# Optimization experiments

Hardware: AMD Instinct MI355X
Metric: run time of the kernel (lower is better)

The kernel has to match this reference:

```python
import jax, jax.numpy as jnp
import numpy as np

N_LETTERS = 256
EMBED_DIM = 1024
HIDDEN_DIM = 2048
SEQ_LEN = 4096


def setup_inputs() -> dict:
    key = jax.random.key(0)
    ks = jax.random.split(key, 8)
    s_e = 1.0 / np.sqrt(EMBED_DIM)
    s_h = 1.0 / np.sqrt(HIDDEN_DIM)
    return {
        "input_ids": jax.random.randint(ks[0], (SEQ_LEN,), 0, N_LETTERS, dtype=jnp.int64)
        if jax.config.jax_enable_x64 else jax.random.randint(ks[0], (SEQ_LEN,), 0, N_LETTERS, dtype=jnp.int32),
        "h0": jnp.zeros((1, 1, HIDDEN_DIM), jnp.float32),
        "c0": jnp.zeros((1, 1, HIDDEN_DIM), jnp.float32),
        "W_emb": jax.random.normal(ks[1], (N_LETTERS, EMBED_DIM), jnp.float32),
        "W_ih": jax.random.normal(ks[2], (4 * HIDDEN_DIM, EMBED_DIM), jnp.float32) * s_e,
        "W_hh": jax.random.normal(ks[3], (4 * HIDDEN_DIM, HIDDEN_DIM), jnp.float32) * s_h,
        "b_ih": jnp.zeros((4 * HIDDEN_DIM,), jnp.float32),
        "b_hh": jnp.zeros((4 * HIDDEN_DIM,), jnp.float32),
        "W_out": jax.random.normal(ks[4], (N_LETTERS, HIDDEN_DIM), jnp.float32) * s_h,
        "b_out": jnp.zeros((N_LETTERS,), jnp.float32),
    }


def reference(input_ids, h0, c0, W_emb, W_ih, W_hh, b_ih, b_hh, W_out, b_out):
    H = W_hh.shape[1]
    emb = W_emb[input_ids]                       # [L, E]
    # Precompute the input-side gate projections for all timesteps (batched GEMM).
    x_gates = emb @ W_ih.T + (b_ih + b_hh)       # [L, 4H]

    def step(carry, xg):
        h, c = carry                             # [H], [H]
        gates = xg + W_hh @ h                    # [4H], PyTorch order i,f,g,o
        i = jax.nn.sigmoid(gates[0 * H:1 * H])
        f = jax.nn.sigmoid(gates[1 * H:2 * H])
        g = jnp.tanh(gates[2 * H:3 * H])
        o = jax.nn.sigmoid(gates[3 * H:4 * H])
        c_new = f * c + i * g
        h_new = o * jnp.tanh(c_new)
        return (h_new, c_new), h_new

    (hL, cL), hs = jax.lax.scan(step, (h0[0, 0], c0[0, 0]), x_gates)  # hs: [L, H]
    logits = hs @ W_out.T + b_out                # [L, n_letters]
    # Dropout(p=0.1) is identity in eval mode.
    out = jax.nn.log_softmax(jax.nn.relu(logits), axis=-1)
    return out, hL[None, None, :], cL[None, None, :]
```

## Files before the change

kernel.cpp:

```cpp
#include <hip/hip_runtime.h>
#include <hip/hip_bf16.h>

#define SEQ 4096
#define EMB 1024
#define HID 2048
#define G4  8192
#define NL  256

typedef __attribute__((ext_vector_type(8))) short bf16x8;
typedef __attribute__((ext_vector_type(4))) float f32x4;

static __device__ __forceinline__ unsigned short f2bf(float f) {
    unsigned int x = __builtin_bit_cast(unsigned int, f);
    return (unsigned short)((x + 0x7FFFu + ((x >> 16) & 1u)) >> 16);
}
static __device__ __forceinline__ float bf2f(unsigned short u) {
    return __builtin_bit_cast(float, ((unsigned int)u) << 16);
}
static __device__ __forceinline__ unsigned long long aload(const unsigned long long* p) {
    return __hip_atomic_load(p, __ATOMIC_RELAXED, __HIP_MEMORY_SCOPE_AGENT);
}
static __device__ __forceinline__ float fsigm(float x) {
    return 1.f / (1.f + __expf(-x));
}
static __device__ __forceinline__ float ftanh(float x) {
    return 1.f - 2.f / (__expf(2.f * x) + 1.f);
}

__global__ __launch_bounds__(256) void k_f2b(const float* __restrict__ in,
                                             unsigned short* __restrict__ out, int n) {
    int i = (blockIdx.x * 256 + threadIdx.x) * 4;
    if (i < n) {
        float4 v = *(const float4*)&in[i];
        ushort4 u;
        u.x = f2bf(v.x); u.y = f2bf(v.y); u.z = f2bf(v.z); u.w = f2bf(v.w);
        *(ushort4*)&out[i] = u;
    }
}

__global__ __launch_bounds__(256) void k_emb(const int* __restrict__ ids,
                                             const float* __restrict__ W_emb,
                                             unsigned short* __restrict__ out) {
    int t = blockIdx.x;
    int e0 = threadIdx.x * 4;
    const float4 v = *(const float4*)&W_emb[(size_t)ids[t] * EMB + e0];
    ushort4 u;
    u.x = f2bf(v.x); u.y = f2bf(v.y); u.z = f2bf(v.z); u.w = f2bf(v.w);
    *(ushort4*)&out[(size_t)t * EMB + e0] = u;
}

#define BM 128
#define BN 128
#define BK 32
__global__ __launch_bounds__(256) void k_gemm_bt(
    const unsigned short* __restrict__ A, const unsigned short* __restrict__ B,
    const float* __restrict__ bias1, const float* __restrict__ bias2,
    float* __restrict__ Cf, unsigned short* __restrict__ Cb,
    int M, int N, int K)
{
    __shared__ unsigned short As[BM * BK];
    __shared__ unsigned short Bs[BN * BK];
    const int bm = blockIdx.x * BM;
    const int bn = blockIdx.y * BN;
    const int tid = threadIdx.x;
    const int wave = tid >> 6, lane = tid & 63;
    const int wm = (wave & 1) * 64, wn = (wave >> 1) * 64;
    const int row16 = lane & 15, quad = lane >> 4;

    f32x4 acc[4][4];
#pragma unroll
    for (int i = 0; i < 4; ++i)
#pragma unroll
        for (int j = 0; j < 4; ++j) acc[i][j] = (f32x4){0.f, 0.f, 0.f, 0.f};

    for (int k0 = 0; k0 < K; k0 += BK) {
        __syncthreads();
#pragma unroll
        for (int s = 0; s < 2; ++s) {
            int c = tid + s * 256;
            int r = c >> 2, col = (c & 3) * 8;
            *(uint4*)&As[r * BK + col] = *(const uint4*)&A[(size_t)(bm + r) * K + k0 + col];
            *(uint4*)&Bs[r * BK + col] = *(const uint4*)&B[(size_t)(bn + r) * K + k0 + col];
        }
        __syncthreads();
        bf16x8 af[4], bfr[4];
#pragma unroll
        for (int i = 0; i < 4; ++i) {
            af[i]  = *(const bf16x8*)&As[(wm + i * 16 + row16) * BK + quad * 8];
            bfr[i] = *(const bf16x8*)&Bs[(wn + i * 16 + row16) * BK + quad * 8];
        }
#pragma unroll
        for (int i = 0; i < 4; ++i)
#pragma unroll
            for (int j = 0; j < 4; ++j)
                acc[i][j] = __builtin_amdgcn_mfma_f32_16x16x32_bf16(af[i], bfr[j], acc[i][j], 0, 0, 0);
    }

#pragma unroll
    for (int j = 0; j < 4; ++j) {
        int col = bn + wn + j * 16 + row16;
        float bsum = (bias1 ? bias1[col] : 0.f) + (bias2 ? bias2[col] : 0.f);
#pragma unroll
        for (int i = 0; i < 4; ++i) {
#pragma unroll
            for (int r = 0; r < 4; ++r) {
                int row = bm + wm + i * 16 + quad * 4 + r;
                float v = acc[i][j][r] + bsum;
                if (Cf) Cf[(size_t)row * N + col] = v;
                else    Cb[(size_t)row * N + col] = f2bf(v);
            }
        }
    }
}

#define LSTM_LDS 90112
__global__ __launch_bounds__(1024, 1) void k_lstm(
    const unsigned short* __restrict__ Whhb,
    const unsigned short* __restrict__ xg,
    const float* __restrict__ h0, const float* __restrict__ c0,
    unsigned short* __restrict__ hsb,
    float* __restrict__ outHC,
    unsigned long long* __restrict__ hcomm)
{
    extern __shared__ char smem[];
    float* LDSp = (float*)smem;

    const int b = blockIdx.x, tid = threadIdx.x;
    const int wave = tid >> 6, lane = tid & 63;
    const int sub = lane & 15, quad = lane >> 4;

    bf16x8 afr[4][4];
#pragma unroll
    for (int q = 0; q < 4; ++q) {
        const unsigned short* wsrc =
            Whhb + ((size_t)(q * HID + b * 16 + sub)) * HID + wave * 128 + quad * 8;
#pragma unroll
        for (int c = 0; c < 4; ++c)
            afr[q][c] = *(const bf16x8*)(wsrc + c * 32);
    }

    float creg = 0.f;
    if (tid < 16) creg = c0[b * 16 + tid];

    for (int t = 0; t < SEQ; ++t) {
        float xq0 = 0.f, xq1 = 0.f, xq2 = 0.f, xq3 = 0.f;
        if (wave == 0 && lane < 16) {
            const unsigned short* xr = xg + (size_t)t * G4 + b * 16 + lane;
            xq0 = bf2f(xr[0]);
            xq1 = bf2f(xr[2048]);
            xq2 = bf2f(xr[4096]);
            xq3 = bf2f(xr[6144]);
        }

        f32x4 acc[4];
#pragma unroll
        for (int q = 0; q < 4; ++q) acc[q] = (f32x4){0.f, 0.f, 0.f, 0.f};

        if (t == 0) {
#pragma unroll
            for (int c = 0; c < 4; ++c) {
                const float* hp = h0 + wave * 128 + c * 32 + quad * 8;
                float4 va = *(const float4*)hp;
                float4 vb = *(const float4*)(hp + 4);
                uint4 d;
                d.x = (unsigned)f2bf(va.x) | ((unsigned)f2bf(va.y) << 16);
                d.y = (unsigned)f2bf(va.z) | ((unsigned)f2bf(va.w) << 16);
                d.z = (unsigned)f2bf(vb.x) | ((unsigned)f2bf(vb.y) << 16);
                d.w = (unsigned)f2bf(vb.z) | ((unsigned)f2bf(vb.w) << 16);
                bf16x8 hf = __builtin_bit_cast(bf16x8, d);
#pragma unroll
                for (int q = 0; q < 4; ++q)
                    acc[q] = __builtin_amdgcn_mfma_f32_16x16x32_bf16(afr[q][c], hf, acc[q], 0, 0, 0);
            }
        } else {
            const unsigned long long* src =
                hcomm + (size_t)((t - 1) & 1) * 8192 + (size_t)(b & 7) * 1024 + wave * 64;
            const unsigned tag = (unsigned)t;
            if (wave != 0) __builtin_amdgcn_s_sleep(10);
            unsigned long long x;
            for (;;) {
                x = aload(&src[lane]);
                if ((unsigned)(x >> 32) == tag) break;
                __builtin_amdgcn_s_sleep(2);
            }
            int myd = (int)(unsigned)x;
#pragma unroll
            for (int c = 0; c < 4; ++c) {
                const int sl = c * 16 + quad * 4;
                uint4 d;
                d.x = (unsigned)__shfl(myd, sl + 0);
                d.y = (unsigned)__shfl(myd, sl + 1);
                d.z = (unsigned)__shfl(myd, sl + 2);
                d.w = (unsigned)__shfl(myd, sl + 3);
                bf16x8 hf = __builtin_bit_cast(bf16x8, d);
#pragma unroll
                for (int q = 0; q < 4; ++q)
                    acc[q] = __builtin_amdgcn_mfma_f32_16x16x32_bf16(afr[q][c], hf, acc[q], 0, 0, 0);
            }
        }

        float* P = LDSp + (t & 1) * 1100;
        if (sub == 0) {
#pragma unroll
            for (int q = 0; q < 4; ++q)
#pragma unroll
                for (int r = 0; r < 4; ++r)
                    P[(q * 16 + quad * 4 + r) * 17 + wave] = acc[q][r];
        }
        __syncthreads();

        if (wave == 0) {
            const float* rp = P + lane * 17;
            float g = 0.f;
#pragma unroll
            for (int i = 0; i < 16; ++i) g += rp[i];
            float gF = __shfl(g, lane + 16);
            float gG = __shfl(g, lane + 32);
            float gO = __shfl(g, lane + 48);
            unsigned hv = 0;
            float cn = 0.f, hn = 0.f;
            if (lane < 16) {
                float gi = g  + xq0;
                float gf = gF + xq1;
                float gg = gG + xq2;
                float go = gO + xq3;
                float i_ = fsigm(gi);
                float f_ = fsigm(gf);
                float g_ = ftanh(gg);
                float o_ = fsigm(go);
                cn = f_ * creg + i_ * g_;
                hn = o_ * ftanh(cn);
                creg = cn;
                hv = (unsigned)f2bf(hn);
            }
            {
                int j8 = lane & 7;
                unsigned lo = (unsigned)__shfl((int)hv, 2 * j8);
                unsigned hi = (unsigned)__shfl((int)hv, 2 * j8 + 1);
                unsigned long long wrd =
                    (((unsigned long long)(unsigned)(t + 1)) << 32)
                    | (unsigned long long)(lo | (hi << 16));
                __hip_atomic_store(
                    &hcomm[(size_t)(t & 1) * 8192 + (size_t)(lane >> 3) * 1024 + b * 8 + j8],
                    wrd, __ATOMIC_RELAXED, __HIP_MEMORY_SCOPE_AGENT);
            }
            if (lane < 16) {
                hsb[(size_t)t * HID + b * 16 + lane] = (unsigned short)hv;
                if (t == SEQ - 1) {
                    outHC[b * 16 + lane] = hn;
                    outHC[HID + b * 16 + lane] = cn;
                }
            }
        }
    }
}

__global__ __launch_bounds__(256) void k_softmax(const float* __restrict__ logits,
                                                 float* __restrict__ out) {
    int row = blockIdx.x * 4 + (threadIdx.x >> 6);
    int lane = threadIdx.x & 63;
    const float* Lr = logits + (size_t)row * NL;
    float4 v = *(const float4*)&Lr[lane * 4];
    v.x = fmaxf(v.x, 0.f); v.y = fmaxf(v.y, 0.f);
    v.z = fmaxf(v.z, 0.f); v.w = fmaxf(v.w, 0.f);
    float m = fmaxf(fmaxf(v.x, v.y), fmaxf(v.z, v.w));
#pragma unroll
    for (int off = 32; off > 0; off >>= 1) m = fmaxf(m, __shfl_xor(m, off));
    float e = __expf(v.x - m) + __expf(v.y - m) + __expf(v.z - m) + __expf(v.w - m);
#pragma unroll
    for (int off = 32; off > 0; off >>= 1) e += __shfl_xor(e, off);
    float ls = __logf(e) + m;
    float4 o;
    o.x = v.x - ls; o.y = v.y - ls; o.z = v.z - ls; o.w = v.w - ls;
    *(float4*)&out[(size_t)row * NL + lane * 4] = o;
}

extern "C" void kernel_launch(void* const* d_in, const int* in_sizes, int n_in,
                              void* d_out, int out_size, void* d_ws, size_t ws_size,
                              hipStream_t stream) {
    const int*   ids   = (const int*)d_in[0];
    const float* h0    = (const float*)d_in[1];
    const float* c0    = (const float*)d_in[2];
    const float* W_emb = (const float*)d_in[3];
    const float* W_ih  = (const float*)d_in[4];
    const float* W_hh  = (const float*)d_in[5];
    const float* b_ih  = (const float*)d_in[6];
    const float* b_hh  = (const float*)d_in[7];
    const float* W_out = (const float*)d_in[8];
    const float* b_out = (const float*)d_in[9];
    float* out = (float*)d_out;

    char* ws = (char*)d_ws;
    unsigned short* xg    = (unsigned short*)(ws);
    unsigned short* hsb   = (unsigned short*)(ws + 67108864);
    unsigned short* Wihb  = (unsigned short*)(ws + 83886080);
    unsigned short* embb  = (unsigned short*)(ws + 100663296);
    unsigned short* Woutb = (unsigned short*)(ws + 109051904);
    float*          logit = (float*)(ws + 110100480);
    unsigned short* Whhb  = (unsigned short*)(ws + 114294784);
    unsigned long long* hcomm = (unsigned long long*)(ws + 147849216);

    k_f2b<<<(G4 * EMB / 4 + 255) / 256, 256, 0, stream>>>(W_ih, Wihb, G4 * EMB);
    k_f2b<<<(NL * HID / 4 + 255) / 256, 256, 0, stream>>>(W_out, Woutb, NL * HID);
    k_f2b<<<(G4 * HID / 4 + 255) / 256, 256, 0, stream>>>(W_hh, Whhb, G4 * HID);
    k_emb<<<SEQ, 256, 0, stream>>>(ids, W_emb, embb);

    dim3 g1(SEQ / BM, G4 / BN);
    k_gemm_bt<<<g1, 256, 0, stream>>>(embb, Wihb, b_ih, b_hh, nullptr, xg, SEQ, G4, EMB);

    hipFuncSetAttribute((const void*)k_lstm, hipFuncAttributeMaxDynamicSharedMemorySize, LSTM_LDS);
    k_lstm<<<128, 1024, LSTM_LDS, stream>>>(Whhb, xg, h0, c0, hsb, out + (size_t)SEQ * NL, hcomm);

    dim3 g2(SEQ / BM, NL / BN);
    k_gemm_bt<<<g2, 256, 0, stream>>>(hsb, Woutb, b_out, nullptr, logit, nullptr, SEQ, NL, HID);

    k_softmax<<<SEQ / 4, 256, 0, stream>>>(logit, out);
}
```

Measured before the change: 10.82 ms.

## Distribute LSTM gate epilogue across all waves and shrink comm words to 32-bit

The per-step gate reduction and cell update now run in all 16 waves, one hidden unit per wave, instead of serially in wave 0. The reduction uses LDS reads plus cross-lane shuffles. The hidden-state exchange packs a 16-bit tag with each bf16 value in a 32-bit word. Readers still load 64-bit pairs and check both tags, which removes the pre-spin sleep and the wave-0 bottleneck on the serial critical path. The cost is redundant transcendental work across lanes, and the 16-bit tag relies on it not wrapping within the double buffer.

New measurement: 15.56 ms. 1.44x slower.

```diff
diff --git a/kernel.cpp b/kernel.cpp
--- a/kernel.cpp
+++ b/kernel.cpp
@@ -19,6 +19,9 @@
 }
 static __device__ __forceinline__ unsigned long long aload(const unsigned long long* p) {
     return __hip_atomic_load(p, __ATOMIC_RELAXED, __HIP_MEMORY_SCOPE_AGENT);
+}
+static __device__ __forceinline__ void astore4(unsigned int* p, unsigned int v) {
+    __hip_atomic_store(p, v, __ATOMIC_RELAXED, __HIP_MEMORY_SCOPE_AGENT);
 }
 static __device__ __forceinline__ float fsigm(float x) {
     return 1.f / (1.f + __expf(-x));
@@ -120,7 +123,7 @@
     const float* __restrict__ h0, const float* __restrict__ c0,
     unsigned short* __restrict__ hsb,
     float* __restrict__ outHC,
-    unsigned long long* __restrict__ hcomm)
+    unsigned int* __restrict__ hcomm)
 {
     extern __shared__ char smem[];
     float* LDSp = (float*)smem;
@@ -139,18 +142,12 @@
             afr[q][c] = *(const bf16x8*)(wsrc + c * 32);
     }
 
-    float creg = 0.f;
-    if (tid < 16) creg = c0[b * 16 + tid];
+    float creg = c0[b * 16 + wave];
 
     for (int t = 0; t < SEQ; ++t) {
-        float xq0 = 0.f, xq1 = 0.f, xq2 = 0.f, xq3 = 0.f;
-        if (wave == 0 && lane < 16) {
-            const unsigned short* xr = xg + (size_t)t * G4 + b * 16 + lane;
-            xq0 = bf2f(xr[0]);
-            xq1 = bf2f(xr[2048]);
-            xq2 = bf2f(xr[4096]);
-            xq3 = bf2f(xr[6144]);
-        }
+        float xqv = 0.f;
+        if (lane < 4)
+            xqv = bf2f(xg[(size_t)t * G4 + lane * 2048 + b * 16 + wave]);
 
         f32x4 acc[4];
 #pragma unroll
@@ -173,17 +170,16 @@
                     acc[q] = __builtin_amdgcn_mfma_f32_16x16x32_bf16(afr[q][c], hf, acc[q], 0, 0, 0);
             }
         } else {
-            const unsigned long long* src =
-                hcomm + (size_t)((t - 1) & 1) * 8192 + (size_t)(b & 7) * 1024 + wave * 64;
-            const unsigned tag = (unsigned)t;
-            if (wave != 0) __builtin_amdgcn_s_sleep(10);
+            const unsigned long long* src = (const unsigned long long*)
+                (hcomm + (size_t)((t - 1) & 1) * 16384 + (size_t)(b & 7) * 2048 + wave * 128);
+            const unsigned tg = (unsigned)t & 0xFFFFu;
             unsigned long long x;
             for (;;) {
                 x = aload(&src[lane]);
-                if ((unsigned)(x >> 32) == tag) break;
-                __builtin_amdgcn_s_sleep(2);
-            }
-            int myd = (int)(unsigned)x;
+                if (((unsigned)x >> 16) == tg && ((unsigned)(x >> 32) >> 16) == tg) break;
+                __builtin_amdgcn_s_sleep(1);
+            }
+            int myd = (int)((((unsigned)(x >> 32)) << 16) | ((unsigned)x & 0xFFFFu));
 #pragma unroll
             for (int c = 0; c < 4; ++c) {
                 const int sl = c * 16 + quad * 4;
@@ -199,7 +195,7 @@
             }
         }
 
-        float* P = LDSp + (t & 1) * 1100;
+        float* P = LDSp + (t & 1) * 1088;
         if (sub == 0) {
 #pragma unroll
             for (int q = 0; q < 4; ++q)
@@ -209,47 +205,30 @@
         }
         __syncthreads();
 
-        if (wave == 0) {
-            const float* rp = P + lane * 17;
-            float g = 0.f;
-#pragma unroll
-            for (int i = 0; i < 16; ++i) g += rp[i];
-            float gF = __shfl(g, lane + 16);
-            float gG = __shfl(g, lane + 32);
-            float gO = __shfl(g, lane + 48);
-            unsigned hv = 0;
-            float cn = 0.f, hn = 0.f;
-            if (lane < 16) {
-                float gi = g  + xq0;
-                float gf = gF + xq1;
-                float gg = gG + xq2;
-                float go = gO + xq3;
-                float i_ = fsigm(gi);
-                float f_ = fsigm(gf);
-                float g_ = ftanh(gg);
-                float o_ = fsigm(go);
-                cn = f_ * creg + i_ * g_;
-                hn = o_ * ftanh(cn);
-                creg = cn;
-                hv = (unsigned)f2bf(hn);
-            }
-            {
-                int j8 = lane & 7;
-                unsigned lo = (unsigned)__shfl((int)hv, 2 * j8);
-                unsigned hi = (unsigned)__shfl((int)hv, 2 * j8 + 1);
-                unsigned long long wrd =
-                    (((unsigned long long)(unsigned)(t + 1)) << 32)
-                    | (unsigned long long)(lo | (hi << 16));
-                __hip_atomic_store(
-                    &hcomm[(size_t)(t & 1) * 8192 + (size_t)(lane >> 3) * 1024 + b * 8 + j8],
-                    wrd, __ATOMIC_RELAXED, __HIP_MEMORY_SCOPE_AGENT);
-            }
-            if (lane < 16) {
-                hsb[(size_t)t * HID + b * 16 + lane] = (unsigned short)hv;
-                if (t == SEQ - 1) {
-                    outHC[b * 16 + lane] = hn;
-                    outHC[HID + b * 16 + lane] = cn;
-                }
+        {
+            float v = P[((lane >> 4) * 16 + wave) * 17 + (lane & 15)];
+            v += __shfl_xor(v, 1); v += __shfl_xor(v, 2);
+            v += __shfl_xor(v, 4); v += __shfl_xor(v, 8);
+            float gi = __shfl(v, 0)  + __shfl(xqv, 0);
+            float gf = __shfl(v, 16) + __shfl(xqv, 1);
+            float gg = __shfl(v, 32) + __shfl(xqv, 2);
+            float go = __shfl(v, 48) + __shfl(xqv, 3);
+            float i_ = fsigm(gi);
+            float f_ = fsigm(gf);
+            float g_ = ftanh(gg);
+            float o_ = fsigm(go);
+            float cn = f_ * creg + i_ * g_;
+            float hn = o_ * ftanh(cn);
+            creg = cn;
+            unsigned hv = (unsigned)f2bf(hn);
+            unsigned wrd = (((unsigned)(t + 1) & 0xFFFFu) << 16) | hv;
+            if (lane < 8)
+                astore4(&hcomm[(size_t)(t & 1) * 16384 + (size_t)lane * 2048 + b * 16 + wave], wrd);
+            if (lane == 8)
+                hsb[(size_t)t * HID + b * 16 + wave] = (unsigned short)hv;
+            if (t == SEQ - 1) {
+                if (lane == 9)  outHC[b * 16 + wave] = hn;
+                if (lane == 10) outHC[HID + b * 16 + wave] = cn;
             }
         }
     }
@@ -298,7 +277,7 @@
     unsigned short* Woutb = (unsigned short*)(ws + 109051904);
     float*          logit = (float*)(ws + 110100480);
     unsigned short* Whhb  = (unsigned short*)(ws + 114294784);
-    unsigned long long* hcomm = (unsigned long long*)(ws + 147849216);
+    unsigned int*   hcomm = (unsigned int*)(ws + 147849216);
 
     k_f2b<<<(G4 * EMB / 4 + 255) / 256, 256, 0, stream>>>(W_ih, Wihb, G4 * EMB);
     k_f2b<<<(NL * HID / 4 + 255) / 256, 256, 0, stream>>>(W_out, Woutb, NL * HID);
```
